# Optimization experiments

Measured on AMD Instinct MI355X. Metric: run time of the kernel, lower is better.

## Reference

```python
import jax, jax.numpy as jnp
import numpy as np

C = 256
K = 8
D = C // K  # qk projection dim = 32


def setup_inputs() -> dict:
    key = jax.random.key(0)
    ks = jax.random.split(key, 9)
    s = 1.0 / np.sqrt(C)
    x = jax.random.normal(ks[0], (4, C, 64, 64), dtype=jnp.float32)
    Wq = jax.random.normal(ks[1], (D, C), dtype=jnp.float32) * s
    bq = jnp.zeros((D,), dtype=jnp.float32)
    Wk = jax.random.normal(ks[2], (D, C), dtype=jnp.float32) * s
    bk = jnp.zeros((D,), dtype=jnp.float32)
    Wv = jax.random.normal(ks[3], (C, C), dtype=jnp.float32) * s
    bv = jnp.zeros((C,), dtype=jnp.float32)
    Wp = jax.random.normal(ks[4], (C, C), dtype=jnp.float32) * s
    bp = jnp.zeros((C,), dtype=jnp.float32)
    gamma = jnp.float32(0.5)  # nonzero so output depends on attention path
    return {"x": x, "Wq": Wq, "bq": bq, "Wk": Wk, "bk": bk,
            "Wv": Wv, "bv": bv, "Wp": Wp, "bp": bp, "gamma": gamma}


def reference(x, Wq, bq, Wk, bk, Wv, bv, Wp, bp, gamma):
    B, Cc, H, W = x.shape
    N = H * W
    xf = x.reshape(B, Cc, N)  # (B, C, N); 1x1 conv == per-pixel linear
    q = jnp.einsum('dc,bcn->bnd', Wq, xf) + bq  # (B, N, D)
    k = jnp.einsum('dc,bcn->bdn', Wk, xf) + bk[None, :, None]  # (B, D, N)
    v = jnp.einsum('dc,bcn->bdn', Wv, xf) + bv[None, :, None]  # (B, C, N)
    scale = 1.0 / jnp.sqrt(jnp.float32(q.shape[-1]))
    attn = jax.nn.softmax(jnp.einsum('bnd,bdm->bnm', q, k) * scale, axis=-1)  # (B, Nq, Nk)
    out = jnp.einsum('bcm,bnm->bcn', v, attn)  # (B, C, Nq)
    out = jnp.einsum('oc,bcn->bon', Wp, out) + bp[None, :, None]
    out = out.reshape(B, Cc, H, W)
    return x + gamma * out
```

## Files before the change

### kernel.cpp

```cpp
#include <hip/hip_runtime.h>
#include <math.h>

#define BB 4
#define CC 256
#define DD 32
#define NN 4096

typedef __attribute__((ext_vector_type(8))) short short8;
typedef __attribute__((ext_vector_type(4))) float floatx4;
typedef __attribute__((ext_vector_type(16))) float floatx16;
typedef __attribute__((ext_vector_type(4))) int intx4;
typedef __attribute__((ext_vector_type(2))) int intx2;

#define SCALEF (0.17677669529663687f * 1.4426950408889634f)

__device__ __forceinline__ ushort f2bf(float f) {
    unsigned int u = __builtin_bit_cast(unsigned int, f);
    u += 0x7FFFu + ((u >> 16) & 1u);
    return (ushort)(u >> 16);
}
__device__ __forceinline__ int pk_trunc(float a, float b) {
    return (int)__builtin_amdgcn_perm(__builtin_bit_cast(unsigned, b),
                                      __builtin_bit_cast(unsigned, a),
                                      0x07060302u);
}
__device__ __forceinline__ float fast_exp2(float x) {
#if __has_builtin(__builtin_amdgcn_exp2f)
    return __builtin_amdgcn_exp2f(x);
#else
    return exp2f(x);
#endif
}
__device__ __forceinline__ void plswap(int& a, int& b) {
#if __has_builtin(__builtin_amdgcn_permlane32_swap)
    intx2 r = __builtin_amdgcn_permlane32_swap(a, b, false, false);
    a = r[0]; b = r[1];
#else
    const int lane = threadIdx.x & 63;
    const bool hi = lane >= 32;
    int a2 = __shfl(a, lane ^ 32);
    int b2 = __shfl(b, lane ^ 32);
    int na = hi ? b2 : a;
    int nb = hi ? b : a2;
    a = na; b = nb;
#endif
}

#define TP 66
__global__ __launch_bounds__(256) void prep_fused(
    const float* __restrict__ x,
    const float* __restrict__ Wq, const float* __restrict__ Wk,
    const float* __restrict__ Wv, const float* __restrict__ Wp,
    ushort* __restrict__ xT, ushort* __restrict__ Wall, ushort* __restrict__ Wpb)
{
    __shared__ ushort tile[64 * TP];
    const int t = threadIdx.x;

    const int bid = (blockIdx.z * gridDim.y + blockIdx.y) * gridDim.x + blockIdx.x;
    if (bid < 144) {
        const int e = (bid * 256 + t) * 4;
        const int row = e >> 8, col = e & 255;
        const float* src;
        float s = 1.0f;
        ushort* dst;
        int drow;
        if (row < 32)       { src = Wq + (size_t)row * CC;          s = SCALEF; dst = Wall; drow = row; }
        else if (row < 64)  { src = Wk + (size_t)(row - 32) * CC;   dst = Wall; drow = row; }
        else if (row < 320) { src = Wv + (size_t)(row - 64) * CC;   dst = Wall; drow = row; }
        else                { src = Wp + (size_t)(row - 320) * CC;  dst = Wpb;  drow = row - 320; }
        const floatx4 w = *(const floatx4*)(src + col);
        int2 d;
        d.x = pk_trunc(w[0] * s, w[1] * s);
        d.y = pk_trunc(w[2] * s, w[3] * s);
        *(int2*)(dst + (size_t)drow * CC + col) = d;
    }

    const int b = blockIdx.z;
    const int c0 = blockIdx.y * 64;
    const int n0 = blockIdx.x * 64;
    const int cl = (t >> 4) * 4;
    const int nl = (t & 15) * 4;

    const float* src = x + ((size_t)b * CC + c0 + cl) * NN + n0 + nl;
    floatx4 v[4];
    #pragma unroll
    for (int i = 0; i < 4; ++i) v[i] = *(const floatx4*)(src + (size_t)i * NN);

    #pragma unroll
    for (int j = 0; j < 4; ++j) {
        *(int*)&tile[(nl + j) * TP + cl]     = pk_trunc(v[0][j], v[1][j]);
        *(int*)&tile[(nl + j) * TP + cl + 2] = pk_trunc(v[2][j], v[3][j]);
    }
    __syncthreads();

    const int nr = t >> 2;
    const int coff = (t & 3) * 16;
    int r[8];
    #pragma unroll
    for (int u = 0; u < 8; ++u) r[u] = *(const int*)&tile[nr * TP + coff + u * 2];
    ushort* dst = xT + ((size_t)b * NN + n0 + nr) * CC + c0 + coff;
    intx4 o0 = {r[0], r[1], r[2], r[3]};
    intx4 o1 = {r[4], r[5], r[6], r[7]};
    *(intx4*)dst = o0;
    *(intx4*)(dst + 8) = o1;
}

__global__ __launch_bounds__(256) void qkv_mfma(
    const ushort* __restrict__ xT, const ushort* __restrict__ Wall,
    const float* __restrict__ bq, const float* __restrict__ bk,
    const float* __restrict__ bv,
    ushort* __restrict__ qb, ushort* __restrict__ kb, ushort* __restrict__ vb)
{
    const int t = threadIdx.x;
    const int wave = t >> 6;
    const int lane = t & 63;
    const int l15 = lane & 15, qd = lane >> 4;
    const int b = blockIdx.z, mt = blockIdx.y;
    const int n0 = blockIdx.x * 128 + wave * 32;

    const ushort* arow = Wall + (size_t)(mt * 32 + l15) * CC + qd * 8;
    const ushort* brow = xT + ((size_t)b * NN + n0 + l15) * CC + qd * 8;

    floatx4 z = {0.f, 0.f, 0.f, 0.f};
    floatx4 acc[2][2];
    acc[0][0] = z; acc[0][1] = z; acc[1][0] = z; acc[1][1] = z;

    #pragma unroll
    for (int k0 = 0; k0 < CC; k0 += 32) {
        short8 af[2], bfr[2];
        af[0]  = *(const short8*)(arow + k0);
        af[1]  = *(const short8*)(arow + 16 * CC + k0);
        bfr[0] = *(const short8*)(brow + k0);
        bfr[1] = *(const short8*)(brow + 16 * CC + k0);
        #pragma unroll
        for (int fm = 0; fm < 2; ++fm)
            #pragma unroll
            for (int fn = 0; fn < 2; ++fn)
                acc[fm][fn] = __builtin_amdgcn_mfma_f32_16x16x32_bf16(af[fm], bfr[fn], acc[fm][fn], 0, 0, 0);
    }

    #pragma unroll
    for (int fm = 0; fm < 2; ++fm) {
        const int o0 = fm * 16 + qd * 4;
        if (mt == 0) {
            const floatx4 bb = *(const floatx4*)(bq + o0);
            #pragma unroll
            for (int fn = 0; fn < 2; ++fn) {
                ushort4 h;
                h.x = f2bf(acc[fm][fn][0] + bb[0] * SCALEF);
                h.y = f2bf(acc[fm][fn][1] + bb[1] * SCALEF);
                h.z = f2bf(acc[fm][fn][2] + bb[2] * SCALEF);
                h.w = f2bf(acc[fm][fn][3] + bb[3] * SCALEF);
                *(ushort4*)(qb + ((size_t)b * NN + n0 + fn * 16 + l15) * DD + o0) = h;
            }
        } else if (mt == 1) {
            const floatx4 bb = *(const floatx4*)(bk + o0);
            #pragma unroll
            for (int fn = 0; fn < 2; ++fn) {
                ushort4 h;
                h.x = f2bf(acc[fm][fn][0] + bb[0]);
                h.y = f2bf(acc[fm][fn][1] + bb[1]);
                h.z = f2bf(acc[fm][fn][2] + bb[2]);
                h.w = f2bf(acc[fm][fn][3] + bb[3]);
                *(ushort4*)(kb + (size_t)b * NN * DD
                                 + (size_t)(n0 / 16 + fn) * 512
                                 + (fm * 2 + (qd >> 1)) * 128
                                 + l15 * 8 + (qd & 1) * 4) = h;
            }
        } else {
            const int oc0 = (mt - 2) * 32 + o0;
            const floatx4 bb = *(const floatx4*)(bv + oc0);
            #pragma unroll
            for (int r = 0; r < 4; ++r)
                #pragma unroll
                for (int fn = 0; fn < 2; ++fn)
                    vb[(size_t)b * CC * NN
                       + (size_t)(n0 / 16 + fn) * (CC * 16)
                       + (oc0 + r) * 16 + l15] = f2bf(acc[fm][fn][r] + bb[r]);
        }
    }
}

__global__ __launch_bounds__(256, 2) void attn_mfma(
    const ushort* __restrict__ qb, const ushort* __restrict__ kb,
    const ushort* __restrict__ vb, ushort* __restrict__ aoT)
{
    __shared__ float red[2][8192];
    __shared__ float lred[2][64];

    const int t = threadIdx.x;
    const int kh = t >> 6;
    const int lane = t & 63;
    const int l31 = lane & 31;
    const bool hi = lane >= 32;
    const int hib = hi ? 8 : 0;
    const int slot = blockIdx.x;
    const int b = slot >> 1;
    const int qt = (slot & 1) * 32 + blockIdx.y;
    const int q0 = qt * 64;
    const int c0 = blockIdx.z * 128;

    short8 qf[2][2];
    #pragma unroll
    for (int qg = 0; qg < 2; ++qg)
        #pragma unroll
        for (int dh = 0; dh < 2; ++dh)
            qf[qg][dh] = *(const short8*)(qb + ((size_t)b * NN + q0 + qg * 32 + l31) * DD + dh * 16 + hib);

    const ushort* krow = kb + (size_t)b * NN * DD + (size_t)kh * 64 * 512
                            + (l31 >> 4) * 512 + (l31 & 15) * 8 + hib * 16;
    const ushort* vrow = vb + (size_t)b * CC * NN + (size_t)kh * 64 * (CC * 16)
                            + (c0 + l31) * 16 + hib;

    floatx16 z16 = {0.f,0.f,0.f,0.f,0.f,0.f,0.f,0.f,0.f,0.f,0.f,0.f,0.f,0.f,0.f,0.f};
    floatx16 acc[2][4];
    #pragma unroll
    for (int qg = 0; qg < 2; ++qg)
        #pragma unroll
        for (int cg = 0; cg < 4; ++cg) acc[qg][cg] = z16;
    float lsum[2] = {0.f, 0.f};

    for (int kt = 0; kt < 32; ++kt) {
        short8 kf0 = *(const short8*)(krow);
        short8 kf1 = *(const short8*)(krow + 256);
        krow += 1024;
        short8 vf[4][2];
        #pragma unroll
        for (int cg = 0; cg < 4; ++cg)
            #pragma unroll
            for (int k2 = 0; k2 < 2; ++k2)
                vf[cg][k2] = *(const short8*)(vrow + cg * 512 + k2 * (CC * 16));
        vrow += 2 * (CC * 16);

        short8 ptB[2][2];
        #pragma unroll
        for (int qg = 0; qg < 2; ++qg) {
            floatx16 s = __builtin_amdgcn_mfma_f32_32x32x16_bf16(kf0, qf[qg][0], z16, 0, 0, 0);
            s = __builtin_amdgcn_mfma_f32_32x32x16_bf16(kf1, qf[qg][1], s, 0, 0, 0);

            float e[16];
            #pragma unroll
            for (int r = 0; r < 16; ++r) e[r] = fast_exp2(s[r]);

            lsum[qg] += (((e[0]+e[1])+(e[2]+e[3]))+((e[4]+e[5])+(e[6]+e[7])))
                      + (((e[8]+e[9])+(e[10]+e[11]))+((e[12]+e[13])+(e[14]+e[15])));

            int a0 = pk_trunc(e[0], e[1]),  b0 = pk_trunc(e[2], e[3]);
            int c0w = pk_trunc(e[4], e[5]), d0 = pk_trunc(e[6], e[7]);
            plswap(a0, c0w);
            plswap(b0, d0);
            intx4 f0 = {a0, b0, c0w, d0};
            ptB[qg][0] = __builtin_bit_cast(short8, f0);

            int a1 = pk_trunc(e[8], e[9]),   b1 = pk_trunc(e[10], e[11]);
            int c1 = pk_trunc(e[12], e[13]), d1 = pk_trunc(e[14], e[15]);
            plswap(a1, c1);
            plswap(b1, d1);
            intx4 f1 = {a1, b1, c1, d1};
            ptB[qg][1] = __builtin_bit_cast(short8, f1);
        }

        __builtin_amdgcn_s_setprio(1);
        #pragma unroll
        for (int cg = 0; cg < 4; ++cg)
            #pragma unroll
            for (int qg = 0; qg < 2; ++qg) {
                acc[qg][cg] = __builtin_amdgcn_mfma_f32_32x32x16_bf16(vf[cg][0], ptB[qg][0], acc[qg][cg], 0, 0, 0);
                acc[qg][cg] = __builtin_amdgcn_mfma_f32_32x32x16_bf16(vf[cg][1], ptB[qg][1], acc[qg][cg], 0, 0, 0);
            }
        __builtin_amdgcn_s_setprio(0);
    }

    #pragma unroll
    for (int qg = 0; qg < 2; ++qg)
        lsum[qg] += __shfl(lsum[qg], lane ^ 32);

    if (kh & 1) {
        const int s = kh >> 1;
        #pragma unroll
        for (int qg = 0; qg < 2; ++qg)
            #pragma unroll
            for (int cg = 0; cg < 4; ++cg)
                #pragma unroll
                for (int r = 0; r < 16; ++r)
                    red[s][((qg * 4 + cg) * 16 + r) * 64 + lane] = acc[qg][cg][r];
        if (!hi)
            #pragma unroll
            for (int qg = 0; qg < 2; ++qg) lred[s][qg * 32 + l31] = lsum[qg];
    }
    __syncthreads();
    if (!(kh & 1)) {
        const int s = kh >> 1;
        #pragma unroll
        for (int qg = 0; qg < 2; ++qg) {
            #pragma unroll
            for (int cg = 0; cg < 4; ++cg)
                #pragma unroll
                for (int r = 0; r < 16; ++r)
                    acc[qg][cg][r] += red[s][((qg * 4 + cg) * 16 + r) * 64 + lane];
            lsum[qg] += lred[s][qg * 32 + l31];
        }
    }
    __syncthreads();
    if (kh == 2) {
        #pragma unroll
        for (int qg = 0; qg < 2; ++qg)
            #pragma unroll
            for (int cg = 0; cg < 4; ++cg)
                #pragma unroll
                for (int r = 0; r < 16; ++r)
                    red[0][((qg * 4 + cg) * 16 + r) * 64 + lane] = acc[qg][cg][r];
        if (!hi)
            #pragma unroll
            for (int qg = 0; qg < 2; ++qg) lred[0][qg * 32 + l31] = lsum[qg];
    }
    __syncthreads();
    if (kh == 0) {
        #pragma unroll
        for (int qg = 0; qg < 2; ++qg) {
            #pragma unroll
            for (int cg = 0; cg < 4; ++cg)
                #pragma unroll
                for (int r = 0; r < 16; ++r)
                    acc[qg][cg][r] += red[0][((qg * 4 + cg) * 16 + r) * 64 + lane];
            lsum[qg] += lred[0][qg * 32 + l31];
        }
        #pragma unroll
        for (int qg = 0; qg < 2; ++qg) {
            const float inv = 1.0f / lsum[qg];
            ushort* dst = aoT + ((size_t)b * NN + q0 + qg * 32 + l31) * CC + c0;
            #pragma unroll
            for (int cg = 0; cg < 4; ++cg) {
                #pragma unroll
                for (int rq = 0; rq < 4; ++rq) {
                    ushort4 h;
                    h.x = f2bf(acc[qg][cg][rq * 4 + 0] * inv);
                    h.y = f2bf(acc[qg][cg][rq * 4 + 1] * inv);
                    h.z = f2bf(acc[qg][cg][rq * 4 + 2] * inv);
                    h.w = f2bf(acc[qg][cg][rq * 4 + 3] * inv);
                    *(ushort4*)(dst + cg * 32 + rq * 8 + (hi ? 4 : 0)) = h;
                }
            }
        }
    }
}

__global__ __launch_bounds__(256) void proj_mfma(
    const ushort* __restrict__ aoT, const ushort* __restrict__ Wpb,
    const float* __restrict__ bp, const float* __restrict__ x,
    const float* __restrict__ gamma, float* __restrict__ out)
{
    const int t = threadIdx.x;
    const int wave = t >> 6;
    const int lane = t & 63;
    const int l15 = lane & 15;
    const int qd = lane >> 4;
    const int b = blockIdx.z;
    const int m0 = blockIdx.y * 32;
    const int n0 = blockIdx.x * 128 + wave * 32;

    floatx4 z = {0.f, 0.f, 0.f, 0.f};
    floatx4 acc[2][2];
    acc[0][0] = z; acc[0][1] = z; acc[1][0] = z; acc[1][1] = z;

    const ushort* arow = aoT + ((size_t)b * NN + n0 + l15) * CC + qd * 8;
    const ushort* wrow = Wpb + (size_t)(m0 + l15) * CC + qd * 8;

    #pragma unroll
    for (int k0 = 0; k0 < CC; k0 += 32) {
        short8 af[2], bfr[2];
        af[0]  = *(const short8*)(wrow + k0);
        af[1]  = *(const short8*)(wrow + 16 * CC + k0);
        bfr[0] = *(const short8*)(arow + k0);
        bfr[1] = *(const short8*)(arow + 16 * CC + k0);
        #pragma unroll
        for (int fm = 0; fm < 2; ++fm)
            #pragma unroll
            for (int fn = 0; fn < 2; ++fn)
                acc[fm][fn] = __builtin_amdgcn_mfma_f32_16x16x32_bf16(af[fm], bfr[fn], acc[fm][fn], 0, 0, 0);
    }

    const float g = gamma[0];
    #pragma unroll
    for (int fm = 0; fm < 2; ++fm) {
        #pragma unroll
        for (int r = 0; r < 4; ++r) {
            int m = m0 + fm * 16 + qd * 4 + r;
            float bpv = bp[m];
            #pragma unroll
            for (int fn = 0; fn < 2; ++fn) {
                size_t addr = ((size_t)b * CC + m) * NN + n0 + fn * 16 + l15;
                out[addr] = fmaf(g, acc[fm][fn][r] + bpv, x[addr]);
            }
        }
    }
}

extern "C" void kernel_launch(void* const* d_in, const int* in_sizes, int n_in,
                              void* d_out, int out_size, void* d_ws, size_t ws_size,
                              hipStream_t stream)
{
    const float* x     = (const float*)d_in[0];
    const float* Wq    = (const float*)d_in[1];
    const float* bq    = (const float*)d_in[2];
    const float* Wk    = (const float*)d_in[3];
    const float* bk    = (const float*)d_in[4];
    const float* Wv    = (const float*)d_in[5];
    const float* bv    = (const float*)d_in[6];
    const float* Wp    = (const float*)d_in[7];
    const float* bp    = (const float*)d_in[8];
    const float* gamma = (const float*)d_in[9];
    float* out = (float*)d_out;

    ushort* qbw  = (ushort*)d_ws;
    ushort* kbw  = qbw + (size_t)BB * NN * DD;
    ushort* vbw  = kbw + (size_t)BB * NN * DD;
    ushort* xaoT = vbw + (size_t)BB * CC * NN;
    ushort* Wall = xaoT + (size_t)BB * NN * CC;
    ushort* Wpb  = Wall + (size_t)320 * CC;

    prep_fused<<<dim3(NN / 64, CC / 64, BB), 256, 0, stream>>>(x, Wq, Wk, Wv, Wp, xaoT, Wall, Wpb);
    qkv_mfma<<<dim3(NN / 128, 10, BB), 256, 0, stream>>>(xaoT, Wall, bq, bk, bv, qbw, kbw, vbw);
    attn_mfma<<<dim3(8, 32, 2), 256, 0, stream>>>(qbw, kbw, vbw, xaoT);
    proj_mfma<<<dim3(NN / 128, CC / 32, BB), 256, 0, stream>>>(xaoT, Wpb, bp, x, gamma, out);
}
```

Measured before the change: 172.9 us.

## Fuse x transpose/convert into QKV projection kernel via shared-memory tile

Merges the prep kernel (x transpose to bf16 and weight conversion) into the QKV projection. Each 640-thread block stages a 64-pixel by 256-channel bf16 tile of x in LDS, and each of its 10 waves computes one 32-row output tile. The waves read fp32 weights and convert them to bf16 on the fly. This removes one launch and the global round trip of the transposed x buffer, at the cost of redundant weight conversion in every block and lower occupancy from the large LDS tile and big blocks.

```diff
diff --git a/kernel.cpp b/kernel.cpp
--- a/kernel.cpp
+++ b/kernel.cpp
@@ -46,96 +46,99 @@
 #endif
 }
 
-#define TP 66
-__global__ __launch_bounds__(256) void prep_fused(
+#define QTP 264
+__global__ __launch_bounds__(640) void qkv_fused(
     const float* __restrict__ x,
-    const float* __restrict__ Wq, const float* __restrict__ Wk,
-    const float* __restrict__ Wv, const float* __restrict__ Wp,
-    ushort* __restrict__ xT, ushort* __restrict__ Wall, ushort* __restrict__ Wpb)
-{
-    __shared__ ushort tile[64 * TP];
-    const int t = threadIdx.x;
-
-    const int bid = (blockIdx.z * gridDim.y + blockIdx.y) * gridDim.x + blockIdx.x;
-    if (bid < 144) {
-        const int e = (bid * 256 + t) * 4;
-        const int row = e >> 8, col = e & 255;
-        const float* src;
-        float s = 1.0f;
-        ushort* dst;
-        int drow;
-        if (row < 32)       { src = Wq + (size_t)row * CC;          s = SCALEF; dst = Wall; drow = row; }
-        else if (row < 64)  { src = Wk + (size_t)(row - 32) * CC;   dst = Wall; drow = row; }
-        else if (row < 320) { src = Wv + (size_t)(row - 64) * CC;   dst = Wall; drow = row; }
-        else                { src = Wp + (size_t)(row - 320) * CC;  dst = Wpb;  drow = row - 320; }
-        const floatx4 w = *(const floatx4*)(src + col);
-        int2 d;
-        d.x = pk_trunc(w[0] * s, w[1] * s);
-        d.y = pk_trunc(w[2] * s, w[3] * s);
-        *(int2*)(dst + (size_t)drow * CC + col) = d;
-    }
-
-    const int b = blockIdx.z;
-    const int c0 = blockIdx.y * 64;
-    const int n0 = blockIdx.x * 64;
-    const int cl = (t >> 4) * 4;
-    const int nl = (t & 15) * 4;
-
-    const float* src = x + ((size_t)b * CC + c0 + cl) * NN + n0 + nl;
-    floatx4 v[4];
-    #pragma unroll
-    for (int i = 0; i < 4; ++i) v[i] = *(const floatx4*)(src + (size_t)i * NN);
-
-    #pragma unroll
-    for (int j = 0; j < 4; ++j) {
-        *(int*)&tile[(nl + j) * TP + cl]     = pk_trunc(v[0][j], v[1][j]);
-        *(int*)&tile[(nl + j) * TP + cl + 2] = pk_trunc(v[2][j], v[3][j]);
-    }
-    __syncthreads();
-
-    const int nr = t >> 2;
-    const int coff = (t & 3) * 16;
-    int r[8];
-    #pragma unroll
-    for (int u = 0; u < 8; ++u) r[u] = *(const int*)&tile[nr * TP + coff + u * 2];
-    ushort* dst = xT + ((size_t)b * NN + n0 + nr) * CC + c0 + coff;
-    intx4 o0 = {r[0], r[1], r[2], r[3]};
-    intx4 o1 = {r[4], r[5], r[6], r[7]};
-    *(intx4*)dst = o0;
-    *(intx4*)(dst + 8) = o1;
-}
-
-__global__ __launch_bounds__(256) void qkv_mfma(
-    const ushort* __restrict__ xT, const ushort* __restrict__ Wall,
-    const float* __restrict__ bq, const float* __restrict__ bk,
-    const float* __restrict__ bv,
+    const float* __restrict__ Wq, const float* __restrict__ bq,
+    const float* __restrict__ Wk, const float* __restrict__ bk,
+    const float* __restrict__ Wv, const float* __restrict__ bv,
+    const float* __restrict__ Wp, ushort* __restrict__ Wpb,
     ushort* __restrict__ qb, ushort* __restrict__ kb, ushort* __restrict__ vb)
 {
+    __shared__ ushort tile[64 * QTP];
+
     const int t = threadIdx.x;
     const int wave = t >> 6;
     const int lane = t & 63;
     const int l15 = lane & 15, qd = lane >> 4;
-    const int b = blockIdx.z, mt = blockIdx.y;
-    const int n0 = blockIdx.x * 128 + wave * 32;
-
-    const ushort* arow = Wall + (size_t)(mt * 32 + l15) * CC + qd * 8;
-    const ushort* brow = xT + ((size_t)b * NN + n0 + l15) * CC + qd * 8;
+    const int b = blockIdx.y;
+    const int n0 = blockIdx.x * 64;
+    const int mt = wave;
+
+    const int bid = blockIdx.y * gridDim.x + blockIdx.x;
+    if (bid < 64 && t < 256) {
+        const int e = (bid * 256 + t) * 4;
+        const int row = e >> 8, col = e & 255;
+        const floatx4 w = *(const floatx4*)(Wp + (size_t)row * CC + col);
+        int2 d;
+        d.x = pk_trunc(w[0], w[1]);
+        d.y = pk_trunc(w[2], w[3]);
+        *(int2*)(Wpb + (size_t)row * CC + col) = d;
+    }
+
+    if (t < 256) {
+        const int cl = (t >> 4) * 4;
+        const int nl = (t & 15) * 4;
+        #pragma unroll
+        for (int p = 0; p < 4; ++p) {
+            const int cp = p * 64;
+            const float* src = x + ((size_t)b * CC + cp + cl) * NN + n0 + nl;
+            floatx4 v[4];
+            #pragma unroll
+            for (int i = 0; i < 4; ++i) v[i] = *(const floatx4*)(src + (size_t)i * NN);
+            #pragma unroll
+            for (int j = 0; j < 4; ++j) {
+                *(int*)&tile[(nl + j) * QTP + cp + cl]     = pk_trunc(v[0][j], v[1][j]);
+                *(int*)&tile[(nl + j) * QTP + cp + cl + 2] = pk_trunc(v[2][j], v[3][j]);
+            }
+        }
+    }
+    __syncthreads();
+
+    const float* wr[2];
+    if (mt == 0) {
+        wr[0] = Wq + (size_t)l15 * CC;
+        wr[1] = Wq + (size_t)(16 + l15) * CC;
+    } else if (mt == 1) {
+        wr[0] = Wk + (size_t)l15 * CC;
+        wr[1] = Wk + (size_t)(16 + l15) * CC;
+    } else {
+        wr[0] = Wv + (size_t)((mt - 2) * 32 + l15) * CC;
+        wr[1] = Wv + (size_t)((mt - 2) * 32 + 16 + l15) * CC;
+    }
 
     floatx4 z = {0.f, 0.f, 0.f, 0.f};
-    floatx4 acc[2][2];
-    acc[0][0] = z; acc[0][1] = z; acc[1][0] = z; acc[1][1] = z;
+    floatx4 acc[2][4];
+    #pragma unroll
+    for (int fm = 0; fm < 2; ++fm)
+        #pragma unroll
+        for (int fn = 0; fn < 4; ++fn) acc[fm][fn] = z;
 
     #pragma unroll
     for (int k0 = 0; k0 < CC; k0 += 32) {
-        short8 af[2], bfr[2];
-        af[0]  = *(const short8*)(arow + k0);
-        af[1]  = *(const short8*)(arow + 16 * CC + k0);
-        bfr[0] = *(const short8*)(brow + k0);
-        bfr[1] = *(const short8*)(brow + 16 * CC + k0);
+        short8 af[2], bfr[4];
+        #pragma unroll
+        for (int f = 0; f < 2; ++f) {
+            const float* p = wr[f] + k0 + qd * 8;
+            float w[8];
+            #pragma unroll
+            for (int j = 0; j < 8; ++j) w[j] = p[j];
+            if (mt == 0) {
+                #pragma unroll
+                for (int j = 0; j < 8; ++j) w[j] *= SCALEF;
+            }
+            intx4 d;
+            d[0] = pk_trunc(w[0], w[1]); d[1] = pk_trunc(w[2], w[3]);
+            d[2] = pk_trunc(w[4], w[5]); d[3] = pk_trunc(w[6], w[7]);
+            af[f] = __builtin_bit_cast(short8, d);
+        }
+        #pragma unroll
+        for (int fn = 0; fn < 4; ++fn)
+            bfr[fn] = *(const short8*)&tile[(fn * 16 + l15) * QTP + k0 + qd * 8];
         #pragma unroll
         for (int fm = 0; fm < 2; ++fm)
             #pragma unroll
-            for (int fn = 0; fn < 2; ++fn)
+            for (int fn = 0; fn < 4; ++fn)
                 acc[fm][fn] = __builtin_amdgcn_mfma_f32_16x16x32_bf16(af[fm], bfr[fn], acc[fm][fn], 0, 0, 0);
     }
 
@@ -145,7 +148,7 @@
         if (mt == 0) {
             const floatx4 bb = *(const floatx4*)(bq + o0);
             #pragma unroll
-            for (int fn = 0; fn < 2; ++fn) {
+            for (int fn = 0; fn < 4; ++fn) {
                 ushort4 h;
                 h.x = f2bf(acc[fm][fn][0] + bb[0] * SCALEF);
                 h.y = f2bf(acc[fm][fn][1] + bb[1] * SCALEF);
@@ -156,7 +159,7 @@
         } else if (mt == 1) {
             const floatx4 bb = *(const floatx4*)(bk + o0);
             #pragma unroll
-            for (int fn = 0; fn < 2; ++fn) {
+            for (int fn = 0; fn < 4; ++fn) {
                 ushort4 h;
                 h.x = f2bf(acc[fm][fn][0] + bb[0]);
                 h.y = f2bf(acc[fm][fn][1] + bb[1]);
@@ -173,7 +176,7 @@
             #pragma unroll
             for (int r = 0; r < 4; ++r)
                 #pragma unroll
-                for (int fn = 0; fn < 2; ++fn)
+                for (int fn = 0; fn < 4; ++fn)
                     vb[(size_t)b * CC * NN
                        + (size_t)(n0 / 16 + fn) * (CC * 16)
                        + (oc0 + r) * 16 + l15] = f2bf(acc[fm][fn][r] + bb[r]);
@@ -412,15 +415,13 @@
     const float* gamma = (const float*)d_in[9];
     float* out = (float*)d_out;
 
-    ushort* qbw  = (ushort*)d_ws;
-    ushort* kbw  = qbw + (size_t)BB * NN * DD;
-    ushort* vbw  = kbw + (size_t)BB * NN * DD;
-    ushort* xaoT = vbw + (size_t)BB * CC * NN;
-    ushort* Wall = xaoT + (size_t)BB * NN * CC;
-    ushort* Wpb  = Wall + (size_t)320 * CC;
-
-    prep_fused<<<dim3(NN / 64, CC / 64, BB), 256, 0, stream>>>(x, Wq, Wk, Wv, Wp, xaoT, Wall, Wpb);
-    qkv_mfma<<<dim3(NN / 128, 10, BB), 256, 0, stream>>>(xaoT, Wall, bq, bk, bv, qbw, kbw, vbw);
-    attn_mfma<<<dim3(8, 32, 2), 256, 0, stream>>>(qbw, kbw, vbw, xaoT);
-    proj_mfma<<<dim3(NN / 128, CC / 32, BB), 256, 0, stream>>>(xaoT, Wpb, bp, x, gamma, out);
-}
+    ushort* qbw = (ushort*)d_ws;
+    ushort* kbw = qbw + (size_t)BB * NN * DD;
+    ushort* vbw = kbw + (size_t)BB * NN * DD;
+    ushort* aoT = vbw + (size_t)BB * CC * NN;
+    ushort* Wpb = aoT + (size_t)BB * NN * CC;
+
+    qkv_fused<<<dim3(NN / 64, BB), 640, 0, stream>>>(x, Wq, bq, Wk, bk, Wv, bv, Wp, Wpb, qbw, kbw, vbw);
+    attn_mfma<<<dim3(8, 32, 2), 256, 0, stream>>>(qbw, kbw, vbw, aoT);
+    proj_mfma<<<dim3(NN / 128, CC / 32, BB), 256, 0, stream>>>(aoT, Wpb, bp, x, gamma, out);
+}
```

After: 162.2 us. -6.2%, faster.
